# Kernel optimization log

Measured on AMD Instinct MI355X. Metric: run time of the kernel, lower is better.

The kernel has to match this reference:

```python
import jax, jax.numpy as jnp
import numpy as np

T = 1024
HID = 2880
H = 64        # query heads
KVH = 8       # kv heads
G = H // KVH  # GQA group size
D = 64        # head dim
WIN = 128     # sliding window
BASE = 150000.0
INIT_CTX = 4096
SCALING = 32.0
NTK_ALPHA = 1.0
NTK_BETA = 32.0
EPS = 1e-5


def _rope_cache():
    # YaRN-style NTK rope cache (scaling_factor > 1 branch), computed in float32.
    d_half = D // 2
    freq = BASE ** (np.arange(0, D, 2, dtype=np.float64) / D)
    concentration = 0.1 * np.log(SCALING) + 1.0
    low = d_half * np.log(INIT_CTX / (NTK_BETA * 2 * np.pi)) / np.log(BASE)
    high = d_half * np.log(INIT_CTX / (NTK_ALPHA * 2 * np.pi)) / np.log(BASE)
    interpolation = 1.0 / (SCALING * freq)
    extrapolation = 1.0 / freq
    ramp = (np.arange(d_half, dtype=np.float64) - low) / (high - low)
    mask = 1.0 - np.clip(ramp, 0.0, 1.0)
    inv_freq = interpolation * (1.0 - mask) + extrapolation * mask
    t = np.arange(INIT_CTX, dtype=np.float64)
    freqs = np.outer(t, inv_freq)                  # [INIT_CTX, D/2]
    cos = (np.cos(freqs) * concentration).astype(np.float32)
    sin = (np.sin(freqs) * concentration).astype(np.float32)
    return jnp.asarray(cos), jnp.asarray(sin)

_COS, _SIN = _rope_cache()


def _apply_rope(x, cos, sin):
    # x: [T, nh, D], cos/sin: [T, D/2]
    c = cos[:, None, :]
    s = sin[:, None, :]
    x1, x2 = jnp.split(x, 2, axis=-1)
    return jnp.concatenate([x1 * c - x2 * s, x2 * c + x1 * s], axis=-1)


def setup_inputs() -> dict:
    key = jax.random.key(0)
    ks = jax.random.split(key, 8)
    hidden_states = jax.random.normal(ks[0], (T, HID), dtype=jnp.float32)
    positions = jnp.arange(T, dtype=jnp.int32)
    norm_scale = jnp.ones((HID,), dtype=jnp.float32)
    qkv_out = H * D + 2 * KVH * D  # 4096 + 512 + 512
    w_qkv = jax.random.normal(ks[1], (HID, qkv_out), dtype=jnp.float32) * (HID ** -0.5)
    b_qkv = jax.random.normal(ks[2], (qkv_out,), dtype=jnp.float32) * 0.01
    w_out = jax.random.normal(ks[3], (H * D, HID), dtype=jnp.float32) * ((H * D) ** -0.5)
    b_out = jax.random.normal(ks[4], (HID,), dtype=jnp.float32) * 0.01
    sinks = jax.random.normal(ks[5], (H,), dtype=jnp.float32)
    return {"hidden_states": hidden_states, "positions": positions,
            "norm_scale": norm_scale, "w_qkv": w_qkv, "b_qkv": b_qkv,
            "w_out": w_out, "b_out": b_out, "sinks": sinks}


def reference(hidden_states, positions, norm_scale, w_qkv, b_qkv, w_out, b_out, sinks):
    # RMSNorm (fp32 math)
    t = hidden_states
    t = t * jax.lax.rsqrt(jnp.mean(t * t, axis=-1, keepdims=True) + EPS)
    t = t * norm_scale

    # fused QKV projection
    qkv = t @ w_qkv + b_qkv
    q = qkv[:, : H * D].reshape(T, H, D)
    k = qkv[:, H * D: H * D + KVH * D].reshape(T, KVH, D)
    v = qkv[:, H * D + KVH * D:].reshape(T, KVH, D)

    # RoPE
    cos = _COS[positions]
    sin = _SIN[positions]
    q = _apply_rope(q, cos, sin)
    k = _apply_rope(k, cos, sin)

    # GQA attention with sliding window + learned sinks
    qg = q.reshape(T, KVH, G, D)
    scale = D ** -0.5
    scores = jnp.einsum('qhgd,khd->hgqk', qg, k) * scale  # [KVH, G, T, T]
    i = jnp.arange(T)[:, None]
    j = jnp.arange(T)[None, :]
    allowed = (j <= i) & (j > i - WIN)  # causal + sliding window
    scores = jnp.where(allowed, scores, -jnp.inf)
    sink = sinks.reshape(KVH, G)[..., None]  # [KVH, G, 1]
    lse = jnp.logaddexp(jax.nn.logsumexp(scores, axis=-1), sink)  # [KVH, G, T]
    probs = jnp.exp(scores - lse[..., None])  # sink mass not attached to any value
    attn = jnp.einsum('hgqk,khd->qhgd', probs, v).reshape(T, H * D)

    out = attn @ w_out + b_out
    return out + hidden_states
```

## Files before the change

kernel.cpp:

```cpp
#include <hip/hip_runtime.h>
#include <hip/hip_bf16.h>
#include <math.h>

#define T_SEQ 1024
#define HIDD 2880
#define NH   64
#define NKVH 8
#define GQ   8
#define HD   64
#define WIN  128
#define QKV_N 5120
#define QDIM  4096
#define KOFF  4096
#define VOFF  4608
#define NPAD_OUT 2944
#define RMS_EPS 1e-5f
#define Z1 3
#define KS1 960
#define Z2 8
#define KS2 512
#define P1SZ (T_SEQ * QKV_N)
#define P2SZ (T_SEQ * HIDD)

typedef __attribute__((ext_vector_type(8))) short short8;
typedef __attribute__((ext_vector_type(4))) short s16x4;
typedef __attribute__((ext_vector_type(4))) float floatx4;

__device__ __forceinline__ float bf2f(unsigned short u) {
    unsigned int x = ((unsigned int)u) << 16;
    float f; __builtin_memcpy(&f, &x, 4); return f;
}
__device__ __forceinline__ unsigned short f2bf(float f) {
    unsigned int x; __builtin_memcpy(&x, &f, 4);
    unsigned int r = (x + 0x7fffu + ((x >> 16) & 1u)) >> 16;
    return (unsigned short)r;
}
__device__ __forceinline__ void glds16(const unsigned short* g, unsigned short* l) {
    __builtin_amdgcn_global_load_lds(
        (const __attribute__((address_space(1))) void*)g,
        (__attribute__((address_space(3))) void*)l, 16, 0, 0);
}

__global__ __launch_bounds__(256) void prep_kernel(
    const float* __restrict__ w_qkv, const float* __restrict__ w_out,
    const float* __restrict__ hidden, const float* __restrict__ norm_scale,
    const int* __restrict__ positions,
    unsigned short* __restrict__ bqkvT, unsigned short* __restrict__ boutT,
    unsigned short* __restrict__ xn,
    float* __restrict__ tabc, float* __restrict__ tabs)
{
    __shared__ unsigned short tile[64 * 66];
    __shared__ float red[4];
    int blk = blockIdx.x;
    int t = threadIdx.x;

    if (blk < 6544) {
        const float* in; unsigned short* out; int R, C, bx, by;
        if (blk < 3600) { in = w_qkv; out = bqkvT; R = HIDD; C = QKV_N; bx = blk % 80; by = blk / 80; }
        else { int r = blk - 3600; in = w_out; out = boutT; R = QDIM; C = HIDD; bx = r % 46; by = r / 46; }
        int r0 = by * 64, c0 = bx * 64;
        bool inr = (c0 < C);
#pragma unroll
        for (int p = 0; p < 4; ++p) {
            int row = p * 16 + (t >> 4);
            int col = (t & 15) * 4;
            float4 v = inr ? *(const float4*)&in[(size_t)(r0 + row) * C + c0 + col]
                           : make_float4(0.f, 0.f, 0.f, 0.f);
            unsigned int w0 = (unsigned)f2bf(v.x) | ((unsigned)f2bf(v.y) << 16);
            unsigned int w1 = (unsigned)f2bf(v.z) | ((unsigned)f2bf(v.w) << 16);
            *(unsigned int*)&tile[row * 66 + col]     = w0;
            *(unsigned int*)&tile[row * 66 + col + 2] = w1;
        }
        __syncthreads();
        int oc = t >> 2, ks = (t & 3) * 16;
        unsigned short vbuf[16];
#pragma unroll
        for (int j = 0; j < 16; ++j) vbuf[j] = tile[(ks + j) * 66 + oc];
        unsigned short* dst = &out[(size_t)(c0 + oc) * R + r0 + ks];
        *(uint4*)dst       = *(uint4*)&vbuf[0];
        *(uint4*)(dst + 8) = *(uint4*)&vbuf[8];
    } else if (blk < 7568) {
        int row = blk - 6544;
        const float4* hr4 = (const float4*)(hidden + (size_t)row * HIDD);
        const float4* sc4 = (const float4*)norm_scale;
        float ss = 0.f;
        for (int i = t; i < HIDD / 4; i += 256) {
            float4 v = hr4[i];
            ss += v.x * v.x + v.y * v.y + v.z * v.z + v.w * v.w;
        }
        for (int m = 32; m; m >>= 1) ss += __shfl_xor(ss, m, 64);
        if ((t & 63) == 0) red[t >> 6] = ss;
        __syncthreads();
        float tot = red[0] + red[1] + red[2] + red[3];
        float r = rsqrtf(tot / (float)HIDD + RMS_EPS);
        uint2* xr = (uint2*)(xn + (size_t)row * HIDD);
        for (int i = t; i < HIDD / 4; i += 256) {
            float4 v = hr4[i], s4 = sc4[i];
            unsigned int lo = (unsigned)f2bf(v.x * r * s4.x) | ((unsigned)f2bf(v.y * r * s4.y) << 16);
            unsigned int hi = (unsigned)f2bf(v.z * r * s4.z) | ((unsigned)f2bf(v.w * r * s4.w) << 16);
            uint2 o; o.x = lo; o.y = hi;
            xr[i] = o;
        }
    } else {
        int idx = (blk - 7568) * 256 + t;
        int tt = idx >> 5, i = idx & 31;
        double freq = pow(150000.0, (double)(2 * i) / 64.0);
        double lnbase = log(150000.0);
        double low  = 32.0 * log(4096.0 / (32.0 * 2.0 * M_PI)) / lnbase;
        double high = 32.0 * log(4096.0 / (2.0 * M_PI)) / lnbase;
        double ramp = ((double)i - low) / (high - low);
        double mask = 1.0 - fmin(fmax(ramp, 0.0), 1.0);
        double invf = (1.0 / (32.0 * freq)) * (1.0 - mask) + (1.0 / freq) * mask;
        double conc = 0.1 * log(32.0) + 1.0;
        double ang = (double)positions[tt] * invf;
        tabc[idx] = (float)(cos(ang) * conc);
        tabs[idx] = (float)(sin(ang) * conc);
    }
}

#define BK 32

template <int MODE>
__global__ __launch_bounds__(256) void gemm_partial_kernel(
    const unsigned short* __restrict__ A, const unsigned short* __restrict__ BT,
    unsigned short* __restrict__ P, int M, int N, int K, int Ks)
{
    int b = blockIdx.x;
    int x, y, z;
    if (MODE == 0) {
        int xg = b & 7; int j = b >> 3;
        int xs = j % 5; int yz = j / 5;
        y = yz & 7; z = yz >> 3; x = xg * 5 + xs;
    } else {
        z = b & 7; int r = b >> 3;
        x = r % 23; y = r / 23;
    }

    __shared__ unsigned short sA[128 * BK];
    __shared__ unsigned short sB[128 * BK];
    int tid = threadIdx.x;
    int m0 = y * 128;
    int n0 = x * 128;
    int kbeg = z * Ks, kend = kbeg + Ks;
    int lane = tid & 63, wave = tid >> 6;
    int wm = (wave & 1) * 64, wn = (wave >> 1) * 64;
    int quad = lane >> 4, l16 = lane & 15;

    floatx4 acc[4][4];
#pragma unroll
    for (int a = 0; a < 4; a++)
#pragma unroll
        for (int bb = 0; bb < 4; bb++) acc[a][bb] = (floatx4){0.f, 0.f, 0.f, 0.f};

    int srow = tid >> 2;
    int kch  = (tid & 3) * 8;
    const unsigned short* gA0 = A  + (size_t)(m0 + srow) * K + kch;
    const unsigned short* gA1 = A  + (size_t)(m0 + 64 + srow) * K + kch;
    const unsigned short* gB0 = BT + (size_t)(n0 + srow) * K + kch;
    const unsigned short* gB1 = BT + (size_t)(n0 + 64 + srow) * K + kch;
    unsigned short* lA0 = sA +        wave * 512 + lane * 8;
    unsigned short* lA1 = sA + 2048 + wave * 512 + lane * 8;
    unsigned short* lB0 = sB +        wave * 512 + lane * 8;
    unsigned short* lB1 = sB + 2048 + wave * 512 + lane * 8;

    for (int k0 = kbeg; k0 < kend; k0 += BK) {
        __syncthreads();
        glds16(gA0 + k0, lA0);
        glds16(gA1 + k0, lA1);
        glds16(gB0 + k0, lB0);
        glds16(gB1 + k0, lB1);
        __syncthreads();

        short8 af[4], bfr[4];
#pragma unroll
        for (int im = 0; im < 4; im++)
            af[im] = *(const short8*)&sA[(wm + im * 16 + l16) * BK + quad * 8];
#pragma unroll
        for (int in = 0; in < 4; in++)
            bfr[in] = *(const short8*)&sB[(wn + in * 16 + l16) * BK + quad * 8];
#pragma unroll
        for (int im = 0; im < 4; im++)
#pragma unroll
            for (int in = 0; in < 4; in++)
                acc[im][in] = __builtin_amdgcn_mfma_f32_16x16x32_bf16(
                    af[im], bfr[in], acc[im][in], 0, 0, 0);
    }

    unsigned short* Pz = P + (size_t)z * M * N;
#pragma unroll
    for (int im = 0; im < 4; im++)
#pragma unroll
        for (int in = 0; in < 4; in++) {
            int col = n0 + wn + in * 16 + l16;
            if (col < N) {
#pragma unroll
                for (int r = 0; r < 4; r++) {
                    int row = m0 + wm + im * 16 + quad * 4 + r;
                    Pz[(size_t)row * N + col] = f2bf(acc[im][in][r]);
                }
            }
        }
}

__global__ __launch_bounds__(256) void reduce_out_kernel(
    const unsigned short* __restrict__ P, const float* __restrict__ bias,
    const float* __restrict__ resid, float* __restrict__ out)
{
    int idx = (blockIdx.x * 256 + threadIdx.x) * 4;
    int n = idx % HIDD;
    float4 rv = *(const float4*)(resid + idx);
    float4 bv = *(const float4*)(bias + n);
    float a0 = bv.x + rv.x, a1 = bv.y + rv.y, a2 = bv.z + rv.z, a3 = bv.w + rv.w;
#pragma unroll
    for (int z = 0; z < Z2; ++z) {
        s16x4 p = *(const s16x4*)(P + (size_t)z * P2SZ + idx);
        a0 += bf2f((unsigned short)p[0]);
        a1 += bf2f((unsigned short)p[1]);
        a2 += bf2f((unsigned short)p[2]);
        a3 += bf2f((unsigned short)p[3]);
    }
    float4 ov = {a0, a1, a2, a3};
    *(float4*)(out + idx) = ov;
}

__global__ __launch_bounds__(512) void attn_kernel(
    const unsigned short* __restrict__ P1, const float* __restrict__ b_qkv,
    const float* __restrict__ sinks,
    const float* __restrict__ tabc, const float* __restrict__ tabs,
    unsigned short* __restrict__ attn)
{
    int i0 = blockIdx.x * 16;
    int kh = blockIdx.y;
    int tid = threadIdx.x, lane = tid & 63, g = tid >> 6;
    int quad = lane >> 4, l16 = lane & 15;
    int tile_j0 = i0 - 127;

    __shared__ unsigned short sU[8 * 16 * 168];
    __shared__ unsigned short sVt[64 * 168];
    unsigned short* sK = sU;
    unsigned short* sPw = sU + g * 16 * 168;

    {
        int d = lane, dd = lane & 31;
        float kb1 = b_qkv[KOFF + kh * 64 + d];
        float kb2 = b_qkv[KOFF + kh * 64 + (d ^ 32)];
        float vb  = b_qkv[VOFF + kh * 64 + d];
        for (int it = 0; it < 18; ++it) {
            int s = it * 8 + g;
            int j = tile_j0 + s;
            unsigned short kst = 0, vst = 0;
            if (j >= 0 && j < T_SEQ) {
                size_t ko = (size_t)j * QKV_N + KOFF + kh * 64;
                float x1 = kb1, x2 = kb2, vv = vb;
#pragma unroll
                for (int z = 0; z < Z1; ++z) {
                    const unsigned short* Pz = P1 + (size_t)z * P1SZ;
                    x1 += bf2f(Pz[ko + d]);
                    x2 += bf2f(Pz[ko + (d ^ 32)]);
                    vv += bf2f(Pz[ko + 512 + d]);
                }
                float c = tabc[j * 32 + dd], sn = tabs[j * 32 + dd];
                kst = f2bf((d < 32) ? (x1 * c - x2 * sn) : (x1 * c + x2 * sn));
                vst = f2bf(vv);
            }
            sK[s * 72 + d] = kst;
            sVt[d * 168 + s] = vst;
        }
        sVt[d * 168 + 144 + 2 * g]     = 0;
        sVt[d * 168 + 144 + 2 * g + 1] = 0;
    }

    int qi = i0 + l16;
    int hb = (kh * GQ + g) * 64;
    short8 qa, qb;
    {
        size_t qo = (size_t)qi * QKV_N + hb + quad * 8;
        float x1[8], x2[8];
#pragma unroll
        for (int j = 0; j < 8; ++j) {
            x1[j] = b_qkv[hb + quad * 8 + j];
            x2[j] = b_qkv[hb + quad * 8 + 32 + j];
        }
#pragma unroll
        for (int z = 0; z < Z1; ++z) {
            const unsigned short* Pz = P1 + (size_t)z * P1SZ;
            short8 lo = *(const short8*)(Pz + qo);
            short8 hi = *(const short8*)(Pz + qo + 32);
#pragma unroll
            for (int j = 0; j < 8; ++j) {
                x1[j] += bf2f((unsigned short)lo[j]);
                x2[j] += bf2f((unsigned short)hi[j]);
            }
        }
        const float* cc = tabc + qi * 32 + quad * 8;
        const float* sc = tabs + qi * 32 + quad * 8;
#pragma unroll
        for (int j = 0; j < 8; ++j) {
            float c = cc[j] * 0.125f, sn = sc[j] * 0.125f;
            qa[j] = (short)f2bf(x1[j] * c - x2[j] * sn);
            qb[j] = (short)f2bf(x2[j] * c + x1[j] * sn);
        }
    }
    __syncthreads();

    floatx4 Sc[9];
#pragma unroll
    for (int nt = 0; nt < 9; ++nt) Sc[nt] = (floatx4){0.f, 0.f, 0.f, 0.f};
#pragma unroll
    for (int nt = 0; nt < 9; ++nt) {
        short8 kb0 = *(const short8*)&sK[(nt * 16 + l16) * 72 + quad * 8];
        short8 kb1 = *(const short8*)&sK[(nt * 16 + l16) * 72 + 32 + quad * 8];
        Sc[nt] = __builtin_amdgcn_mfma_f32_16x16x32_bf16(qa, kb0, Sc[nt], 0, 0, 0);
        Sc[nt] = __builtin_amdgcn_mfma_f32_16x16x32_bf16(qb, kb1, Sc[nt], 0, 0, 0);
    }

    int smin = 127 - i0;
    float mx[4], sm[4], inv[4];
#pragma unroll
    for (int r = 0; r < 4; ++r) {
        int qoff = quad * 4 + r;
        int lo = qoff > smin ? qoff : smin;
        int hi = qoff + 127;
        float m = -INFINITY;
#pragma unroll
        for (int nt = 0; nt < 9; ++nt) {
            int s = nt * 16 + l16;
            float v = (s >= lo && s <= hi) ? Sc[nt][r] : -INFINITY;
            Sc[nt][r] = v;
            m = fmaxf(m, v);
        }
        mx[r] = m;
    }
#pragma unroll
    for (int mmask = 1; mmask < 16; mmask <<= 1)
#pragma unroll
        for (int r = 0; r < 4; ++r)
            mx[r] = fmaxf(mx[r], __shfl_xor(mx[r], mmask, 64));
    float sink = sinks[kh * GQ + g];
#pragma unroll
    for (int r = 0; r < 4; ++r) {
        mx[r] = fmaxf(mx[r], sink);
        float s = 0.f;
#pragma unroll
        for (int nt = 0; nt < 9; ++nt) {
            float p = __expf(Sc[nt][r] - mx[r]);
            Sc[nt][r] = p;
            s += p;
        }
        sm[r] = s;
    }
#pragma unroll
    for (int mmask = 1; mmask < 16; mmask <<= 1)
#pragma unroll
        for (int r = 0; r < 4; ++r)
            sm[r] += __shfl_xor(sm[r], mmask, 64);
#pragma unroll
    for (int r = 0; r < 4; ++r)
        inv[r] = 1.f / (sm[r] + __expf(sink - mx[r]));

    __syncthreads();

#pragma unroll
    for (int nt = 0; nt < 9; ++nt)
#pragma unroll
        for (int r = 0; r < 4; ++r)
            sPw[(quad * 4 + r) * 168 + nt * 16 + l16] = f2bf(Sc[nt][r]);
    {
        int q = lane >> 2, so = (lane & 3) * 4;
        *(s16x4*)&sPw[q * 168 + 144 + so] = (s16x4){0, 0, 0, 0};
    }

    floatx4 O[4];
#pragma unroll
    for (int nt = 0; nt < 4; ++nt) O[nt] = (floatx4){0.f, 0.f, 0.f, 0.f};
#pragma unroll
    for (int kt = 0; kt < 5; ++kt) {
        short8 pa = *(const short8*)&sPw[l16 * 168 + kt * 32 + quad * 8];
#pragma unroll
        for (int nt = 0; nt < 4; ++nt) {
            short8 vb = *(const short8*)&sVt[(nt * 16 + l16) * 168 + kt * 32 + quad * 8];
            O[nt] = __builtin_amdgcn_mfma_f32_16x16x32_bf16(pa, vb, O[nt], 0, 0, 0);
        }
    }
#pragma unroll
    for (int nt = 0; nt < 4; ++nt)
#pragma unroll
        for (int r = 0; r < 4; ++r) {
            int q = quad * 4 + r;
            attn[(size_t)(i0 + q) * QDIM + (kh * GQ + g) * 64 + nt * 16 + l16] =
                f2bf(O[nt][r] * inv[r]);
        }
}

extern "C" void kernel_launch(void* const* d_in, const int* in_sizes, int n_in,
                              void* d_out, int out_size, void* d_ws, size_t ws_size,
                              hipStream_t stream)
{
    const float* hidden     = (const float*)d_in[0];
    const int*   positions  = (const int*)d_in[1];
    const float* norm_scale = (const float*)d_in[2];
    const float* w_qkv      = (const float*)d_in[3];
    const float* b_qkv      = (const float*)d_in[4];
    const float* w_out      = (const float*)d_in[5];
    const float* b_out      = (const float*)d_in[6];
    const float* sinks      = (const float*)d_in[7];
    float* out = (float*)d_out;

    char* ws = (char*)d_ws;
    float*          tabc  = (float*)ws;
    float*          tabs  = (float*)(ws + 131072);
    unsigned short* attnb = (unsigned short*)(ws + 262144);
    unsigned short* boutT = (unsigned short*)(ws + 8650752);
    unsigned short* xn    = (unsigned short*)(ws + 32768000);
    unsigned short* bqkvT = (unsigned short*)(ws + 38666240);
    unsigned short* P1    = (unsigned short*)(ws + 68157440);
    unsigned short* P2    = (unsigned short*)(ws + 38666240);

    prep_kernel<<<7696, 256, 0, stream>>>(
        w_qkv, w_out, hidden, norm_scale, positions, bqkvT, boutT, xn, tabc, tabs);
    gemm_partial_kernel<0><<<40 * 8 * Z1, 256, 0, stream>>>(
        xn, bqkvT, P1, T_SEQ, QKV_N, HIDD, KS1);
    attn_kernel<<<dim3(T_SEQ / 16, NKVH), 512, 0, stream>>>(
        P1, b_qkv, sinks, tabc, tabs, attnb);
    gemm_partial_kernel<1><<<23 * 8 * Z2, 256, 0, stream>>>(
        attnb, boutT, P2, T_SEQ, HIDD, QDIM, KS2);
    reduce_out_kernel<<<2880, 256, 0, stream>>>(P2, b_out, hidden, out);
}
```

Measured before the change: 283.1 us.

## Replace split-K GEMMs with 256x256 tiled double-buffered pipelined MFMA kernel

Replaces the 128x128, BK=32 split-K GEMM with a 256x256-tile, 512-thread kernel. It uses swizzled LDS, a double-buffered 64-wide K pipeline built on global_load_lds, explicit vmcnt waits and setprio around the MFMA phases. The output GEMM's split-K drops from 8 to 4, and the w_out transpose is padded to 3072 columns so 256-wide tiles fit; the workspace layout is reshuffled to match. The goal is more data reuse per tile, fewer barriers per FLOP and less partial-sum traffic. The cost is fewer blocks (240 and 192), which may underfill the CUs, plus heavier register and LDS pressure.

```diff
diff --git a/kernel.cpp b/kernel.cpp
--- a/kernel.cpp
+++ b/kernel.cpp
@@ -13,12 +13,12 @@
 #define QDIM  4096
 #define KOFF  4096
 #define VOFF  4608
-#define NPAD_OUT 2944
+#define NPAD_OUT 3072
 #define RMS_EPS 1e-5f
 #define Z1 3
 #define KS1 960
-#define Z2 8
-#define KS2 512
+#define Z2 4
+#define KS2 1024
 #define P1SZ (T_SEQ * QKV_N)
 #define P2SZ (T_SEQ * HIDD)
 
@@ -54,10 +54,10 @@
     int blk = blockIdx.x;
     int t = threadIdx.x;
 
-    if (blk < 6544) {
+    if (blk < 6672) {
         const float* in; unsigned short* out; int R, C, bx, by;
         if (blk < 3600) { in = w_qkv; out = bqkvT; R = HIDD; C = QKV_N; bx = blk % 80; by = blk / 80; }
-        else { int r = blk - 3600; in = w_out; out = boutT; R = QDIM; C = HIDD; bx = r % 46; by = r / 46; }
+        else { int r = blk - 3600; in = w_out; out = boutT; R = QDIM; C = HIDD; bx = r % 48; by = r / 48; }
         int r0 = by * 64, c0 = bx * 64;
         bool inr = (c0 < C);
 #pragma unroll
@@ -79,8 +79,8 @@
         unsigned short* dst = &out[(size_t)(c0 + oc) * R + r0 + ks];
         *(uint4*)dst       = *(uint4*)&vbuf[0];
         *(uint4*)(dst + 8) = *(uint4*)&vbuf[8];
-    } else if (blk < 7568) {
-        int row = blk - 6544;
+    } else if (blk < 7696) {
+        int row = blk - 6672;
         const float4* hr4 = (const float4*)(hidden + (size_t)row * HIDD);
         const float4* sc4 = (const float4*)norm_scale;
         float ss = 0.f;
@@ -102,7 +102,7 @@
             xr[i] = o;
         }
     } else {
-        int idx = (blk - 7568) * 256 + t;
+        int idx = (blk - 7696) * 256 + t;
         int tt = idx >> 5, i = idx & 31;
         double freq = pow(150000.0, (double)(2 * i) / 64.0);
         double lnbase = log(150000.0);
@@ -118,87 +118,159 @@
     }
 }
 
-#define BK 32
-
-template <int MODE>
-__global__ __launch_bounds__(256) void gemm_partial_kernel(
+
+#define SYNCPRE() do { \
+    __builtin_amdgcn_s_barrier(); \
+    asm volatile("s_waitcnt lgkmcnt(0)"); \
+    __builtin_amdgcn_s_setprio(1); \
+} while (0)
+#define SYNCPOST() do { \
+    __builtin_amdgcn_s_setprio(0); \
+    __builtin_amdgcn_s_barrier(); \
+} while (0)
+
+#define LDA_FRAGS(SLOT, QM) do { \
+    const unsigned short* _pa = lds + ((SLOT)*4 + (QM)) * 8192 + rowA * 64; \
+    _Pragma("unroll") \
+    for (int _t = 0; _t < 4; ++_t) { \
+        af[_t][0] = *(const short8*)(_pa + _t * 1024 + sl0); \
+        af[_t][1] = *(const short8*)(_pa + _t * 1024 + sl1); \
+    } \
+} while (0)
+
+#define LDB_FRAGS(SLOT, QN, BF) do { \
+    const unsigned short* _pb = lds + ((SLOT)*4 + 2 + (QN)) * 8192 + rowB * 64; \
+    _Pragma("unroll") \
+    for (int _u = 0; _u < 2; ++_u) { \
+        BF[_u][0] = *(const short8*)(_pb + _u * 1024 + sl0); \
+        BF[_u][1] = *(const short8*)(_pb + _u * 1024 + sl1); \
+    } \
+} while (0)
+
+#define MFMA_Q(QM, QN, BF) do { \
+    _Pragma("unroll") \
+    for (int _t = 0; _t < 4; ++_t) { \
+        _Pragma("unroll") \
+        for (int _u = 0; _u < 2; ++_u) { \
+            floatx4 _c = acc[QM][_t][QN][_u]; \
+            _c = __builtin_amdgcn_mfma_f32_16x16x32_bf16(af[_t][0], BF[_u][0], _c, 0, 0, 0); \
+            _c = __builtin_amdgcn_mfma_f32_16x16x32_bf16(af[_t][1], BF[_u][1], _c, 0, 0, 0); \
+            acc[QM][_t][QN][_u] = _c; \
+        } \
+    } \
+} while (0)
+
+#define STAGE(SLOT, MAT, HALF, GP, GR0, KT) do { \
+    unsigned short* _d = lds + ((SLOT)*4 + (MAT)*2 + (HALF)) * 8192 + stdst; \
+    const unsigned short* _s = (GP) + (size_t)((GR0) + (HALF)*128 + st_r0) * K + kbeg + (KT)*64 + st_c0; \
+    glds16(_s, _d); \
+    glds16(_s + (size_t)8 * K, _d + 512); \
+} while (0)
+
+template <int NX>
+__global__ __launch_bounds__(512, 2) void gemm256_kernel(
     const unsigned short* __restrict__ A, const unsigned short* __restrict__ BT,
     unsigned short* __restrict__ P, int M, int N, int K, int Ks)
 {
+    __shared__ unsigned short lds[65536];
+
     int b = blockIdx.x;
-    int x, y, z;
-    if (MODE == 0) {
-        int xg = b & 7; int j = b >> 3;
-        int xs = j % 5; int yz = j / 5;
-        y = yz & 7; z = yz >> 3; x = xg * 5 + xs;
-    } else {
-        z = b & 7; int r = b >> 3;
-        x = r % 23; y = r / 23;
-    }
-
-    __shared__ unsigned short sA[128 * BK];
-    __shared__ unsigned short sB[128 * BK];
+    int cpx = (int)gridDim.x >> 3;
+    int sid = (b & 7) * cpx + (b >> 3);
+    int y = sid & 3;
+    int xz = sid >> 2;
+    int x = xz % NX, z = xz / NX;
+    int m0 = y * 256, n0 = x * 256;
+    int kbeg = z * Ks;
+    int NT = Ks >> 6;
+    int NIT = NT >> 1;
+
     int tid = threadIdx.x;
-    int m0 = y * 128;
-    int n0 = x * 128;
-    int kbeg = z * Ks, kend = kbeg + Ks;
-    int lane = tid & 63, wave = tid >> 6;
-    int wm = (wave & 1) * 64, wn = (wave >> 1) * 64;
-    int quad = lane >> 4, l16 = lane & 15;
-
-    floatx4 acc[4][4];
-#pragma unroll
-    for (int a = 0; a < 4; a++)
-#pragma unroll
-        for (int bb = 0; bb < 4; bb++) acc[a][bb] = (floatx4){0.f, 0.f, 0.f, 0.f};
-
-    int srow = tid >> 2;
-    int kch  = (tid & 3) * 8;
-    const unsigned short* gA0 = A  + (size_t)(m0 + srow) * K + kch;
-    const unsigned short* gA1 = A  + (size_t)(m0 + 64 + srow) * K + kch;
-    const unsigned short* gB0 = BT + (size_t)(n0 + srow) * K + kch;
-    const unsigned short* gB1 = BT + (size_t)(n0 + 64 + srow) * K + kch;
-    unsigned short* lA0 = sA +        wave * 512 + lane * 8;
-    unsigned short* lA1 = sA + 2048 + wave * 512 + lane * 8;
-    unsigned short* lB0 = sB +        wave * 512 + lane * 8;
-    unsigned short* lB1 = sB + 2048 + wave * 512 + lane * 8;
-
-    for (int k0 = kbeg; k0 < kend; k0 += BK) {
-        __syncthreads();
-        glds16(gA0 + k0, lA0);
-        glds16(gA1 + k0, lA1);
-        glds16(gB0 + k0, lB0);
-        glds16(gB1 + k0, lB1);
-        __syncthreads();
-
-        short8 af[4], bfr[4];
-#pragma unroll
-        for (int im = 0; im < 4; im++)
-            af[im] = *(const short8*)&sA[(wm + im * 16 + l16) * BK + quad * 8];
-#pragma unroll
-        for (int in = 0; in < 4; in++)
-            bfr[in] = *(const short8*)&sB[(wn + in * 16 + l16) * BK + quad * 8];
-#pragma unroll
-        for (int im = 0; im < 4; im++)
-#pragma unroll
-            for (int in = 0; in < 4; in++)
-                acc[im][in] = __builtin_amdgcn_mfma_f32_16x16x32_bf16(
-                    af[im], bfr[in], acc[im][in], 0, 0, 0);
+    int ln = tid & 63, wv = tid >> 6;
+    int l16 = ln & 15, quad = ln >> 4;
+    int wm = wv >> 2, wn = wv & 3;
+    int e8 = l16 & 7;
+    int sl0 = ((quad ^ e8) << 3);
+    int sl1 = (((4 + quad) ^ e8) << 3);
+    int rowA = wm * 64 + l16;
+    int rowB = wn * 32 + l16;
+    int st_r0 = (wv << 4) + (ln >> 3);
+    int st_c0 = (((ln & 7) ^ ((ln >> 3) & 7)) << 3);
+    int stdst = (wv << 10) + (ln << 3);
+
+    short8 af[4][2], b0[2][2], b1[2][2];
+    floatx4 acc[2][4][2][2];
+#pragma unroll
+    for (int qm = 0; qm < 2; ++qm)
+#pragma unroll
+        for (int t = 0; t < 4; ++t)
+#pragma unroll
+            for (int qn = 0; qn < 2; ++qn)
+#pragma unroll
+                for (int u = 0; u < 2; ++u)
+                    acc[qm][t][qn][u] = (floatx4){0.f, 0.f, 0.f, 0.f};
+
+    STAGE(0, 0, 0, A,  m0, 0); STAGE(0, 0, 1, A,  m0, 0);
+    STAGE(0, 1, 0, BT, n0, 0); STAGE(0, 1, 1, BT, n0, 0);
+    STAGE(1, 0, 0, A,  m0, 1); STAGE(1, 1, 0, BT, n0, 1);
+    asm volatile("s_waitcnt vmcnt(0)");
+    __builtin_amdgcn_s_barrier();
+
+    int a = 0;
+    for (int i = 0; i < NIT; ++i, a += 2) {
+        bool k2 = (a + 2) < NT, k3 = (a + 3) < NT;
+        LDA_FRAGS(0, 0); LDB_FRAGS(0, 0, b0);
+        STAGE(1, 1, 1, BT, n0, a + 1); STAGE(1, 0, 1, A, m0, a + 1);
+        SYNCPRE(); MFMA_Q(0, 0, b0); SYNCPOST();
+        LDB_FRAGS(0, 1, b1);
+        SYNCPRE(); MFMA_Q(0, 1, b1); SYNCPOST();
+        LDA_FRAGS(0, 1);
+        if (k2) STAGE(0, 0, 0, A, m0, a + 2);
+        SYNCPRE(); MFMA_Q(1, 0, b0); SYNCPOST();
+        if (k2) { STAGE(0, 1, 0, BT, n0, a + 2); asm volatile("s_waitcnt vmcnt(8)"); }
+        else    { asm volatile("s_waitcnt vmcnt(4)"); }
+        SYNCPRE(); MFMA_Q(1, 1, b1); SYNCPOST();
+        LDA_FRAGS(1, 0); LDB_FRAGS(1, 0, b0);
+        if (k2) { STAGE(0, 1, 1, BT, n0, a + 2); STAGE(0, 0, 1, A, m0, a + 2);
+                  asm volatile("s_waitcnt vmcnt(8)"); }
+        else    { asm volatile("s_waitcnt vmcnt(0)"); }
+        SYNCPRE(); MFMA_Q(0, 0, b0); SYNCPOST();
+        LDB_FRAGS(1, 1, b1);
+        SYNCPRE(); MFMA_Q(0, 1, b1); SYNCPOST();
+        LDA_FRAGS(1, 1);
+        if (k3) STAGE(1, 0, 0, A, m0, a + 3);
+        SYNCPRE(); MFMA_Q(1, 0, b0); SYNCPOST();
+        if (k3) { STAGE(1, 1, 0, BT, n0, a + 3); asm volatile("s_waitcnt vmcnt(4)"); }
+        else    { asm volatile("s_waitcnt vmcnt(0)"); }
+        SYNCPRE(); MFMA_Q(1, 1, b1); SYNCPOST();
+    }
+    if (NT & 1) {
+        LDA_FRAGS(0, 0); LDB_FRAGS(0, 0, b0);
+        SYNCPRE(); MFMA_Q(0, 0, b0); SYNCPOST();
+        LDB_FRAGS(0, 1, b1);
+        SYNCPRE(); MFMA_Q(0, 1, b1); SYNCPOST();
+        LDA_FRAGS(0, 1);
+        SYNCPRE(); MFMA_Q(1, 0, b0); SYNCPOST();
+        SYNCPRE(); MFMA_Q(1, 1, b1); SYNCPOST();
     }
 
     unsigned short* Pz = P + (size_t)z * M * N;
 #pragma unroll
-    for (int im = 0; im < 4; im++)
-#pragma unroll
-        for (int in = 0; in < 4; in++) {
-            int col = n0 + wn + in * 16 + l16;
-            if (col < N) {
-#pragma unroll
-                for (int r = 0; r < 4; r++) {
-                    int row = m0 + wm + im * 16 + quad * 4 + r;
-                    Pz[(size_t)row * N + col] = f2bf(acc[im][in][r]);
+    for (int qm = 0; qm < 2; ++qm)
+#pragma unroll
+        for (int t = 0; t < 4; ++t) {
+            int rbase = m0 + qm * 128 + wm * 64 + t * 16 + quad * 4;
+#pragma unroll
+            for (int qn = 0; qn < 2; ++qn)
+#pragma unroll
+                for (int u = 0; u < 2; ++u) {
+                    int col = n0 + qn * 128 + wn * 32 + u * 16 + l16;
+                    if (col < N) {
+#pragma unroll
+                        for (int r = 0; r < 4; ++r)
+                            Pz[(size_t)(rbase + r) * N + col] = f2bf(acc[qm][t][qn][u][r]);
+                    }
                 }
-            }
         }
 }
 
@@ -409,20 +481,20 @@
     char* ws = (char*)d_ws;
     float*          tabc  = (float*)ws;
     float*          tabs  = (float*)(ws + 131072);
-    unsigned short* attnb = (unsigned short*)(ws + 262144);
-    unsigned short* boutT = (unsigned short*)(ws + 8650752);
-    unsigned short* xn    = (unsigned short*)(ws + 32768000);
-    unsigned short* bqkvT = (unsigned short*)(ws + 38666240);
-    unsigned short* P1    = (unsigned short*)(ws + 68157440);
-    unsigned short* P2    = (unsigned short*)(ws + 38666240);
-
-    prep_kernel<<<7696, 256, 0, stream>>>(
+    unsigned short* boutT = (unsigned short*)(ws + 262144);
+    unsigned short* xn    = (unsigned short*)(ws + 25427968);
+    unsigned short* bqkvT = (unsigned short*)(ws + 31326208);
+    unsigned short* P1    = (unsigned short*)(ws + 60817408);
+    unsigned short* attnb = (unsigned short*)(ws + 25427968);
+    unsigned short* P2    = (unsigned short*)(ws + 60817408);
+
+    prep_kernel<<<7824, 256, 0, stream>>>(
         w_qkv, w_out, hidden, norm_scale, positions, bqkvT, boutT, xn, tabc, tabs);
-    gemm_partial_kernel<0><<<40 * 8 * Z1, 256, 0, stream>>>(
+    gemm256_kernel<20><<<4 * 20 * Z1, 512, 0, stream>>>(
         xn, bqkvT, P1, T_SEQ, QKV_N, HIDD, KS1);
     attn_kernel<<<dim3(T_SEQ / 16, NKVH), 512, 0, stream>>>(
         P1, b_qkv, sinks, tabc, tabs, attnb);
-    gemm_partial_kernel<1><<<23 * 8 * Z2, 256, 0, stream>>>(
+    gemm256_kernel<12><<<4 * 12 * Z2, 512, 0, stream>>>(
         attnb, boutT, P2, T_SEQ, HIDD, QDIM, KS2);
     reduce_out_kernel<<<2880, 256, 0, stream>>>(P2, b_out, hidden, out);
 }
```

Result: faster. 254.9 us (-10.0%).
